# Optimization experiments

Hardware: AMD Instinct MI355X
Metric: run time of the kernel (lower is better)

Reference implementation:

```python
import jax, jax.numpy as jnp
import numpy as np

EPS = 1e-8
NUM_HEADS = 4


def setup_inputs() -> dict:
    key = jax.random.key(0)
    ks = jax.random.split(key, 20)
    N, D = 8192, 200      # total nodes, gnn/text dim
    B = 4                  # graphs (text batch)
    E, DEG = 4096, 16      # hyperedges, nodes per hyperedge
    H = 128                # fusion hidden dim
    f = lambda k, s: jax.random.normal(k, s, dtype=jnp.float32) * 0.05
    return {
        "x": jax.random.normal(ks[0], (N, D), dtype=jnp.float32),
        "text": jax.random.normal(ks[1], (B, D), dtype=jnp.float32),
        "W": f(ks[2], (D, D)),
        "b": jnp.zeros((D,), jnp.float32),
        "gate_w": f(ks[3], (D, 1)),
        "gate_b": jnp.zeros((1,), jnp.float32),
        "gnn_w": f(ks[4], (D, H)), "gnn_b": f(ks[5], (H,)),
        "text_w": f(ks[6], (D, H)), "text_b": f(ks[7], (H,)),
        "in_w": f(ks[8], (H, 3 * H)), "in_b": f(ks[9], (3 * H,)),
        "attn_out_w": f(ks[10], (H, H)), "attn_out_b": f(ks[11], (H,)),
        "fgate_w": f(ks[12], (2 * H, H)), "fgate_b": f(ks[13], (H,)),
        "outp_w": f(ks[14], (H, D)), "outp_b": f(ks[15], (D,)),
        "edge_nodes": jax.random.randint(ks[16], (E, DEG), 0, N),
    }


def _forward(x, text, W, b, gate_w, gate_b, gnn_w, gnn_b, text_w, text_b,
             in_w, in_b, attn_out_w, attn_out_b, fgate_w, fgate_b,
             outp_w, outp_b, edge_nodes):
    N, D = x.shape
    E, DEG = edge_nodes.shape
    # --- HypergraphConv: incidence build + normalized Laplacian propagation ---
    out = x @ W                                         # [N, D]
    # H[node, edge] = 1/len(edge); duplicates overwrite (set), as in torch loop
    Hinc = jnp.zeros((N, E), x.dtype).at[edge_nodes, jnp.arange(E)[:, None]].set(1.0 / DEG)
    Dv = Hinc.sum(axis=1)                               # node degree [N]
    De = Hinc.sum(axis=0)                               # edge degree [E]
    dv = 1.0 / jnp.sqrt(Dv + EPS)
    de = 1.0 / (De + EPS)
    Hl = Hinc * dv[:, None]                             # Dv^-1/2 H
    L = (Hl * de[None, :]) @ Hl.T                       # Dv^-1/2 H De^-1 H^T Dv^-1/2
    hyper_out = L @ out                                 # [N, D]
    alpha = jax.nn.sigmoid(x.mean(axis=0, keepdims=True) @ gate_w + gate_b)  # [1,1]
    gnn_feat = alpha * out + (1.0 - alpha) * hyper_out + b
    # --- CrossModalAttentionFusion on per-graph node features (3D path) ---
    B = text.shape[0]
    Nn = N // B
    gnn3 = gnn_feat.reshape(B, Nn, D)
    gp = gnn3 @ gnn_w + gnn_b                           # [B, Nn, H]
    tp = (text @ text_w + text_b)[:, None, :]           # [B, 1, H]
    Hd = gp.shape[-1]
    hd = Hd // NUM_HEADS
    q = gp @ in_w[:, :Hd] + in_b[:Hd]
    k = tp @ in_w[:, Hd:2 * Hd] + in_b[Hd:2 * Hd]
    v = tp @ in_w[:, 2 * Hd:] + in_b[2 * Hd:]
    qh = q.reshape(B, Nn, NUM_HEADS, hd).transpose(0, 2, 1, 3)   # [B,h,Nn,hd]
    kh = k.reshape(B, 1, NUM_HEADS, hd).transpose(0, 2, 1, 3)    # [B,h,1,hd]
    vh = v.reshape(B, 1, NUM_HEADS, hd).transpose(0, 2, 1, 3)
    scores = jnp.einsum("bhqd,bhkd->bhqk", qh, kh) / jnp.sqrt(jnp.float32(hd))
    attn = jax.nn.softmax(scores, axis=-1)              # kv_len=1 -> ones
    att = jnp.einsum("bhqk,bhkd->bhqd", attn, vh)
    att = att.transpose(0, 2, 1, 3).reshape(B, Nn, Hd) @ attn_out_w + attn_out_b
    g = jax.nn.sigmoid(jnp.concatenate([gp, att], axis=-1) @ fgate_w + fgate_b)
    fused = g * gp + (1.0 - g) * att
    return fused @ outp_w + outp_b                      # [B, Nn, D]


def reference(x, text, W, b, gate_w, gate_b, gnn_w, gnn_b, text_w, text_b,
              in_w, in_b, attn_out_w, attn_out_b, fgate_w, fgate_b,
              outp_w, outp_b, edge_nodes):
    return _forward(x, text, W, b, gate_w, gate_b, gnn_w, gnn_b, text_w, text_b,
                    in_w, in_b, attn_out_w, attn_out_b, fgate_w, fgate_b,
                    outp_w, outp_b, edge_nodes)
```

## Files before the change

kernel.cpp:

```cpp
#include <hip/hip_runtime.h>
#include <hip/hip_bf16.h>

#define NODES 8192
#define DIM   200
#define NEDGE 4096
#define DEGREE 16
#define NB    4
#define NNODE 2048
#define HD    128
#define MT    8
#define ECAP  32

__device__ __forceinline__ float dv_of(int cnt) {
    return 1.0f / sqrtf((float)cnt * (1.0f / 16.0f) + 1e-8f);
}

__global__ void k_front(const float* __restrict__ x, const int* __restrict__ en,
                        const float* __restrict__ W, const float* __restrict__ gnn_w,
                        const float* __restrict__ bias, const float* __restrict__ gnn_b,
                        const float* __restrict__ text, const float* __restrict__ text_w,
                        const float* __restrict__ text_b, const float* __restrict__ in_w,
                        const float* __restrict__ in_b, const float* __restrict__ aow,
                        const float* __restrict__ aob, const float* __restrict__ fgw,
                        const float* __restrict__ fgb, float* __restrict__ colsum,
                        int* __restrict__ cnt, int* __restrict__ emask,
                        int* __restrict__ elist2, float* __restrict__ Wg,
                        float* __restrict__ bg, float* __restrict__ attO,
                        float* __restrict__ attg) {
    __shared__ float st[DIM];
    __shared__ float part[2][HD];
    __shared__ float vin[HD];
    int b = blockIdx.x, t = threadIdx.x;
    if (b < 256) {
        if (t < DIM) {
            float acc = 0.f;
            int r0 = b * 32;
            for (int r = 0; r < 32; r++) acc += x[(r0 + r) * DIM + t];
            atomicAdd(&colsum[t], acc);
        }
        return;
    }
    if (b < 272) {
        int e = (b - 256) * 256 + t;
        int idx[DEGREE];
#pragma unroll
        for (int i = 0; i < DEGREE; i++) idx[i] = en[e * DEGREE + i];
        int mask = 0;
#pragma unroll
        for (int i = 0; i < DEGREE; i++) {
            bool uniq = true;
            for (int j = 0; j < i; j++) uniq = uniq && (idx[j] != idx[i]);
            if (uniq) {
                mask |= (1 << i);
                int slot = atomicAdd(&cnt[idx[i]], 1);
                if (slot < ECAP) elist2[idx[i] * ECAP + slot] = e;
            }
        }
        emask[e] = mask;
        return;
    }
    if (b < 372) {
        int r = 2 * (b - 272) + (t >> 7);
        int c = t & 127;
        const float* vec = &W[r * DIM];
        float acc = 0.f;
        for (int k = 0; k < DIM; k++) acc += vec[k] * gnn_w[k * HD + c];
        Wg[r * HD + c] = acc;
        return;
    }
    if (b == 372) {
        if (t < HD) {
            float acc = 0.f;
            for (int k = 0; k < DIM; k++) acc += bias[k] * gnn_w[k * HD + t];
            bg[t] = acc + gnn_b[t];
        }
        return;
    }
    int g = b - 373;
    int c = t & 127, h = t >> 7;
    if (t < DIM) st[t] = text[g * DIM + t];
    __syncthreads();
    {
        float acc = 0.f;
        int k0 = h * 100;
        for (int k = k0; k < k0 + 100; k++) acc += st[k] * text_w[k * HD + c];
        part[h][c] = acc;
    }
    __syncthreads();
    if (t < HD) vin[t] = part[0][t] + part[1][t] + text_b[t];
    __syncthreads();
    {
        float acc = 0.f;
        int k0 = h * 64;
        for (int k = k0; k < k0 + 64; k++) acc += vin[k] * in_w[k * 3 * HD + 2 * HD + c];
        part[h][c] = acc;
    }
    __syncthreads();
    if (t < HD) vin[t] = part[0][t] + part[1][t] + in_b[2 * HD + t];
    __syncthreads();
    {
        float acc = 0.f;
        int k0 = h * 64;
        for (int k = k0; k < k0 + 64; k++) acc += vin[k] * aow[k * HD + c];
        part[h][c] = acc;
    }
    __syncthreads();
    if (t < HD) {
        float ao = part[0][t] + part[1][t] + aob[t];
        attO[g * HD + t] = ao;
        vin[t] = ao;
    }
    __syncthreads();
    {
        float acc = 0.f;
        int k0 = h * 64;
        for (int k = k0; k < k0 + 64; k++) acc += vin[k] * fgw[(HD + k) * HD + c];
        part[h][c] = acc;
    }
    __syncthreads();
    if (t < HD) attg[g * HD + t] = part[0][t] + part[1][t] + fgb[t];
}

__global__ void k_xwg(const float* __restrict__ x, const float* __restrict__ Wg,
                      float* __restrict__ out2, const float* __restrict__ colsum,
                      const float* __restrict__ gate_w, const float* __restrict__ gate_b,
                      float* __restrict__ alpha) {
    __shared__ float sx[MT * DIM];
    int t = threadIdx.x;
    if (blockIdx.x == NODES / MT) {
        __shared__ float red[256];
        red[t] = (t < DIM) ? colsum[t] * gate_w[t] : 0.f;
        __syncthreads();
        for (int o = 128; o > 0; o >>= 1) {
            if (t < o) red[t] += red[t + o];
            __syncthreads();
        }
        if (t == 0) {
            float z = red[0] / (float)NODES + gate_b[0];
            alpha[0] = 1.0f / (1.0f + expf(-z));
        }
        return;
    }
    int bm = blockIdx.x * MT;
    const float4* x4 = (const float4*)(x + bm * DIM);
    float4* sx4 = (float4*)sx;
    for (int i = t; i < MT * DIM / 4; i += 256) sx4[i] = x4[i];
    __syncthreads();
    int c = t & 127, rg = t >> 7;
    float acc[4] = {0.f, 0.f, 0.f, 0.f};
    for (int k = 0; k < DIM; k++) {
        float w = Wg[k * HD + c];
#pragma unroll
        for (int i = 0; i < 4; i++) acc[i] += sx[(rg * 4 + i) * DIM + k] * w;
    }
#pragma unroll
    for (int i = 0; i < 4; i++) out2[(bm + rg * 4 + i) * HD + c] = acc[i];
}

__global__ void k_tE(const int* __restrict__ en, const int* __restrict__ emask,
                     const int* __restrict__ cnt, const float* __restrict__ out2,
                     float* __restrict__ tE) {
    int e = blockIdx.x * 2 + (threadIdx.x >> 7);
    int c = threadIdx.x & 127;
    int m = emask[e];
    float De = (float)__popc(m) * (1.0f / 16.0f);
    float de = 1.0f / (De + 1e-8f);
    int nd[DEGREE];
#pragma unroll
    for (int i = 0; i < DEGREE; i++) nd[i] = en[e * DEGREE + i];
    float acc = 0.f;
#pragma unroll
    for (int i = 0; i < DEGREE; i++)
        if ((m >> i) & 1) acc += dv_of(cnt[nd[i]]) * out2[nd[i] * HD + c];
    tE[e * HD + c] = de * acc;
}

__global__ void k_tail(const float* __restrict__ out2, const float* __restrict__ tE,
                       const int* __restrict__ cnt, const int* __restrict__ elist2,
                       const float* __restrict__ alpha, const float* __restrict__ bg,
                       const float* __restrict__ fgw, const float* __restrict__ attO,
                       const float* __restrict__ attg, const float* __restrict__ opw,
                       const float* __restrict__ opb, float* __restrict__ out) {
    __shared__ float sgp[MT][HD];
    __shared__ int   sid[MT][ECAP];
    __shared__ int   scount[MT];
    int bm = blockIdx.x * MT;
    int b = bm >> 11;
    int t = threadIdx.x;
    {
        int r = t >> 5, sl = t & 31;
        int n = bm + r;
        int cc = cnt[n]; cc = cc < ECAP ? cc : ECAP;
        if (sl == 0) scount[r] = cc;
        if (sl < cc) sid[r][sl] = elist2[n * ECAP + sl];
    }
    __syncthreads();
    int c = t & 127, rg = t >> 7;
    float a = alpha[0];
    float bgc = bg[c];
#pragma unroll
    for (int i = 0; i < 4; i++) {
        int r = rg * 4 + i;
        int n = bm + r;
        int cc = scount[r];
        float hyp = 0.f;
        for (int j = 0; j < cc; j++) hyp += tE[sid[r][j] * HD + c];
        hyp *= dv_of(cnt[n]) * (1.0f / 256.0f);
        sgp[r][c] = a * out2[n * HD + c] + (1.0f - a) * hyp + bgc;
    }
    __syncthreads();
    float ao = attO[b * HD + c];
    float ag = attg[b * HD + c];
    float acc[4] = {ag, ag, ag, ag};
    for (int j = 0; j < HD; j++) {
        float w = fgw[j * HD + c];
#pragma unroll
        for (int i = 0; i < 4; i++) acc[i] += sgp[rg * 4 + i][j] * w;
    }
    __syncthreads();
#pragma unroll
    for (int i = 0; i < 4; i++) {
        int r = rg * 4 + i;
        float g = 1.0f / (1.0f + expf(-acc[i]));
        sgp[r][c] = g * sgp[r][c] + (1.0f - g) * ao;
    }
    __syncthreads();
    if (t < DIM) {
        float accO[MT];
        float ob = opb[t];
#pragma unroll
        for (int i = 0; i < MT; i++) accO[i] = ob;
        for (int j = 0; j < HD; j++) {
            float w = opw[j * DIM + t];
#pragma unroll
            for (int i = 0; i < MT; i++) accO[i] += sgp[i][j] * w;
        }
#pragma unroll
        for (int i = 0; i < MT; i++) out[(bm + i) * DIM + t] = accO[i];
    }
}

extern "C" void kernel_launch(void* const* d_in, const int* in_sizes, int n_in,
                              void* d_out, int out_size, void* d_ws, size_t ws_size,
                              hipStream_t stream) {
    const float* x      = (const float*)d_in[0];
    const float* text   = (const float*)d_in[1];
    const float* W      = (const float*)d_in[2];
    const float* bias   = (const float*)d_in[3];
    const float* gate_w = (const float*)d_in[4];
    const float* gate_b = (const float*)d_in[5];
    const float* gnn_w  = (const float*)d_in[6];
    const float* gnn_b  = (const float*)d_in[7];
    const float* text_w = (const float*)d_in[8];
    const float* text_b = (const float*)d_in[9];
    const float* in_w   = (const float*)d_in[10];
    const float* in_b   = (const float*)d_in[11];
    const float* aow    = (const float*)d_in[12];
    const float* aob    = (const float*)d_in[13];
    const float* fgw    = (const float*)d_in[14];
    const float* fgb    = (const float*)d_in[15];
    const float* opw    = (const float*)d_in[16];
    const float* opb    = (const float*)d_in[17];
    const int*   en     = (const int*)d_in[18];
    float* out = (float*)d_out;

    char* p = (char*)d_ws;
    int*   cnt    = (int*)p;   p += NODES * sizeof(int);
    float* colsum = (float*)p; p += DIM * sizeof(float);
    float* out2   = (float*)p; p += (size_t)NODES * HD * sizeof(float);
    float* tE     = (float*)p; p += (size_t)NEDGE * HD * sizeof(float);
    int*   elist2 = (int*)p;   p += (size_t)NODES * ECAP * sizeof(int);
    float* Wg     = (float*)p; p += DIM * HD * sizeof(float);
    float* alpha  = (float*)p; p += sizeof(float);
    float* bg     = (float*)p; p += HD * sizeof(float);
    float* attO   = (float*)p; p += NB * HD * sizeof(float);
    float* attg   = (float*)p; p += NB * HD * sizeof(float);
    int*   emask  = (int*)p;   p += NEDGE * sizeof(int);

    hipMemsetAsync(cnt, 0, (NODES + DIM) * sizeof(int), stream);

    k_front<<<377, 256, 0, stream>>>(x, en, W, gnn_w, bias, gnn_b, text, text_w,
                                     text_b, in_w, in_b, aow, aob, fgw, fgb,
                                     colsum, cnt, emask, elist2, Wg, bg, attO, attg);
    k_xwg<<<NODES / MT + 1, 256, 0, stream>>>(x, Wg, out2, colsum, gate_w, gate_b, alpha);
    k_tE<<<NEDGE / 2, 256, 0, stream>>>(en, emask, cnt, out2, tE);
    k_tail<<<NODES / MT, 256, 0, stream>>>(out2, tE, cnt, elist2, alpha, bg, fgw,
                                           attO, attg, opw, opb, out);
}
```

Measured before the change: 168.5 us.

## Fuse four kernels into one persistent kernel with global atomic barriers

Replaces the four separate launches with a single persistent kernel of 512 blocks that walks through the stages and separates them with software grid barriers built on agent-scope atomics. The cnt array is now zeroed inside the kernel. colsum atomics are replaced by per-block partial sums that block 0 reduces. Each block handles two node tiles and eight edges per stage. The aim is to remove launch gaps and the larger memset, at the cost of barrier spin overhead and a dependence on all 512 blocks being resident at once.

```diff
diff --git a/kernel.cpp b/kernel.cpp
--- a/kernel.cpp
+++ b/kernel.cpp
@@ -1,50 +1,132 @@
 #include <hip/hip_runtime.h>
-#include <hip/hip_bf16.h>
 
 #define NODES 8192
 #define DIM   200
 #define NEDGE 4096
 #define DEGREE 16
-#define NB    4
-#define NNODE 2048
 #define HD    128
 #define MT    8
 #define ECAP  32
+#define NBLK  512
+#define NTILE (NODES / MT)
+
+struct Params {
+    const float *x, *text, *W, *bias, *gate_w, *gate_b, *gnn_w, *gnn_b,
+                *text_w, *text_b, *in_w, *in_b, *aow, *aob, *fgw, *fgb,
+                *opw, *opb;
+    const int  *en;
+    float *out;
+    int   *bar;
+    int   *cnt;
+    float *cpart;
+    float *out2;
+    float *tE;
+    int   *elist2;
+    float *Wg;
+    float *alpha;
+    float *bg;
+    float *attO;
+    float *attg;
+    int   *emask;
+};
 
 __device__ __forceinline__ float dv_of(int cnt) {
     return 1.0f / sqrtf((float)cnt * (1.0f / 16.0f) + 1e-8f);
 }
 
-__global__ void k_front(const float* __restrict__ x, const int* __restrict__ en,
-                        const float* __restrict__ W, const float* __restrict__ gnn_w,
-                        const float* __restrict__ bias, const float* __restrict__ gnn_b,
-                        const float* __restrict__ text, const float* __restrict__ text_w,
-                        const float* __restrict__ text_b, const float* __restrict__ in_w,
-                        const float* __restrict__ in_b, const float* __restrict__ aow,
-                        const float* __restrict__ aob, const float* __restrict__ fgw,
-                        const float* __restrict__ fgb, float* __restrict__ colsum,
-                        int* __restrict__ cnt, int* __restrict__ emask,
-                        int* __restrict__ elist2, float* __restrict__ Wg,
-                        float* __restrict__ bg, float* __restrict__ attO,
-                        float* __restrict__ attg) {
-    __shared__ float st[DIM];
-    __shared__ float part[2][HD];
-    __shared__ float vin[HD];
-    int b = blockIdx.x, t = threadIdx.x;
+__device__ __forceinline__ void gbar(int* bar, int idx) {
+    __syncthreads();
+    if (threadIdx.x == 0) {
+        __hip_atomic_fetch_add(&bar[idx], 1, __ATOMIC_RELEASE, __HIP_MEMORY_SCOPE_AGENT);
+        while (__hip_atomic_load(&bar[idx], __ATOMIC_RELAXED, __HIP_MEMORY_SCOPE_AGENT) < NBLK)
+            __builtin_amdgcn_s_sleep(2);
+    }
+    __syncthreads();
+    __threadfence();
+}
+
+__global__ __launch_bounds__(256, 4) void k_fused(Params p) {
+    __shared__ __align__(16) union SM {
+        float sx[MT * DIM];
+        struct { float st[DIM]; float part[2][HD]; float vin[HD]; } tx;
+        struct { float sgp[MT][HD]; int sid[MT][ECAP]; int scount[MT]; } tl;
+    } sm;
+    __shared__ float red[256];
+    const int b = blockIdx.x, t = threadIdx.x;
+
+    if (t < 16) p.cnt[b * 16 + t] = 0;
     if (b < 256) {
         if (t < DIM) {
             float acc = 0.f;
             int r0 = b * 32;
-            for (int r = 0; r < 32; r++) acc += x[(r0 + r) * DIM + t];
-            atomicAdd(&colsum[t], acc);
-        }
-        return;
-    }
-    if (b < 272) {
-        int e = (b - 256) * 256 + t;
+            for (int r = 0; r < 32; r++) acc += p.x[(r0 + r) * DIM + t];
+            p.cpart[b * DIM + t] = acc;
+        }
+    } else if (b < 356) {
+        int r = 2 * (b - 256) + (t >> 7), c = t & 127;
+        const float* vec = &p.W[r * DIM];
+        float acc = 0.f;
+        for (int k = 0; k < DIM; k++) acc += vec[k] * p.gnn_w[k * HD + c];
+        p.Wg[r * HD + c] = acc;
+    } else if (b == 356) {
+        if (t < HD) {
+            float acc = 0.f;
+            for (int k = 0; k < DIM; k++) acc += p.bias[k] * p.gnn_w[k * HD + t];
+            p.bg[t] = acc + p.gnn_b[t];
+        }
+    } else if (b < 361) {
+        int g = b - 357;
+        int c = t & 127, h = t >> 7;
+        if (t < DIM) sm.tx.st[t] = p.text[g * DIM + t];
+        __syncthreads();
+        {
+            float acc = 0.f;
+            int k0 = h * 100;
+            for (int k = k0; k < k0 + 100; k++) acc += sm.tx.st[k] * p.text_w[k * HD + c];
+            sm.tx.part[h][c] = acc;
+        }
+        __syncthreads();
+        if (t < HD) sm.tx.vin[t] = sm.tx.part[0][t] + sm.tx.part[1][t] + p.text_b[t];
+        __syncthreads();
+        {
+            float acc = 0.f;
+            int k0 = h * 64;
+            for (int k = k0; k < k0 + 64; k++)
+                acc += sm.tx.vin[k] * p.in_w[k * 3 * HD + 2 * HD + c];
+            sm.tx.part[h][c] = acc;
+        }
+        __syncthreads();
+        if (t < HD) sm.tx.vin[t] = sm.tx.part[0][t] + sm.tx.part[1][t] + p.in_b[2 * HD + t];
+        __syncthreads();
+        {
+            float acc = 0.f;
+            int k0 = h * 64;
+            for (int k = k0; k < k0 + 64; k++) acc += sm.tx.vin[k] * p.aow[k * HD + c];
+            sm.tx.part[h][c] = acc;
+        }
+        __syncthreads();
+        if (t < HD) {
+            float ao = sm.tx.part[0][t] + sm.tx.part[1][t] + p.aob[t];
+            p.attO[g * HD + t] = ao;
+            sm.tx.vin[t] = ao;
+        }
+        __syncthreads();
+        {
+            float acc = 0.f;
+            int k0 = h * 64;
+            for (int k = k0; k < k0 + 64; k++) acc += sm.tx.vin[k] * p.fgw[(HD + k) * HD + c];
+            sm.tx.part[h][c] = acc;
+        }
+        __syncthreads();
+        if (t < HD) p.attg[g * HD + t] = sm.tx.part[0][t] + sm.tx.part[1][t] + p.fgb[t];
+    }
+    gbar(p.bar, 0);
+
+    if (t < 8) {
+        int e = b * 8 + t;
         int idx[DEGREE];
 #pragma unroll
-        for (int i = 0; i < DEGREE; i++) idx[i] = en[e * DEGREE + i];
+        for (int i = 0; i < DEGREE; i++) idx[i] = p.en[e * DEGREE + i];
         int mask = 0;
 #pragma unroll
         for (int i = 0; i < DEGREE; i++) {
@@ -52,238 +134,164 @@
             for (int j = 0; j < i; j++) uniq = uniq && (idx[j] != idx[i]);
             if (uniq) {
                 mask |= (1 << i);
-                int slot = atomicAdd(&cnt[idx[i]], 1);
-                if (slot < ECAP) elist2[idx[i] * ECAP + slot] = e;
+                int slot = atomicAdd(&p.cnt[idx[i]], 1);
+                if (slot < ECAP) p.elist2[idx[i] * ECAP + slot] = e;
             }
         }
-        emask[e] = mask;
-        return;
-    }
-    if (b < 372) {
-        int r = 2 * (b - 272) + (t >> 7);
-        int c = t & 127;
-        const float* vec = &W[r * DIM];
-        float acc = 0.f;
-        for (int k = 0; k < DIM; k++) acc += vec[k] * gnn_w[k * HD + c];
-        Wg[r * HD + c] = acc;
-        return;
-    }
-    if (b == 372) {
-        if (t < HD) {
-            float acc = 0.f;
-            for (int k = 0; k < DIM; k++) acc += bias[k] * gnn_w[k * HD + t];
-            bg[t] = acc + gnn_b[t];
-        }
-        return;
-    }
-    int g = b - 373;
-    int c = t & 127, h = t >> 7;
-    if (t < DIM) st[t] = text[g * DIM + t];
-    __syncthreads();
-    {
-        float acc = 0.f;
-        int k0 = h * 100;
-        for (int k = k0; k < k0 + 100; k++) acc += st[k] * text_w[k * HD + c];
-        part[h][c] = acc;
-    }
-    __syncthreads();
-    if (t < HD) vin[t] = part[0][t] + part[1][t] + text_b[t];
-    __syncthreads();
-    {
-        float acc = 0.f;
-        int k0 = h * 64;
-        for (int k = k0; k < k0 + 64; k++) acc += vin[k] * in_w[k * 3 * HD + 2 * HD + c];
-        part[h][c] = acc;
-    }
-    __syncthreads();
-    if (t < HD) vin[t] = part[0][t] + part[1][t] + in_b[2 * HD + t];
-    __syncthreads();
-    {
-        float acc = 0.f;
-        int k0 = h * 64;
-        for (int k = k0; k < k0 + 64; k++) acc += vin[k] * aow[k * HD + c];
-        part[h][c] = acc;
-    }
-    __syncthreads();
-    if (t < HD) {
-        float ao = part[0][t] + part[1][t] + aob[t];
-        attO[g * HD + t] = ao;
-        vin[t] = ao;
-    }
-    __syncthreads();
-    {
-        float acc = 0.f;
-        int k0 = h * 64;
-        for (int k = k0; k < k0 + 64; k++) acc += vin[k] * fgw[(HD + k) * HD + c];
-        part[h][c] = acc;
-    }
-    __syncthreads();
-    if (t < HD) attg[g * HD + t] = part[0][t] + part[1][t] + fgb[t];
-}
-
-__global__ void k_xwg(const float* __restrict__ x, const float* __restrict__ Wg,
-                      float* __restrict__ out2, const float* __restrict__ colsum,
-                      const float* __restrict__ gate_w, const float* __restrict__ gate_b,
-                      float* __restrict__ alpha) {
-    __shared__ float sx[MT * DIM];
-    int t = threadIdx.x;
-    if (blockIdx.x == NODES / MT) {
-        __shared__ float red[256];
-        red[t] = (t < DIM) ? colsum[t] * gate_w[t] : 0.f;
+        p.emask[e] = mask;
+    }
+    for (int it = 0; it < 2; ++it) {
+        int bm = (b + it * NBLK) * MT;
+        const float4* x4 = (const float4*)(p.x + bm * DIM);
+        float4* sx4 = (float4*)sm.sx;
+        for (int i = t; i < MT * DIM / 4; i += 256) sx4[i] = x4[i];
+        __syncthreads();
+        int c = t & 127, rg = t >> 7;
+        float acc[4] = {0.f, 0.f, 0.f, 0.f};
+        for (int k = 0; k < DIM; k++) {
+            float w = p.Wg[k * HD + c];
+#pragma unroll
+            for (int i = 0; i < 4; i++) acc[i] += sm.sx[(rg * 4 + i) * DIM + k] * w;
+        }
+#pragma unroll
+        for (int i = 0; i < 4; i++) p.out2[(bm + rg * 4 + i) * HD + c] = acc[i];
+        __syncthreads();
+    }
+    if (b == 0) {
+        float v = 0.f;
+        if (t < DIM) {
+            float s = 0.f;
+            for (int q = 0; q < 256; q++) s += p.cpart[q * DIM + t];
+            v = s * p.gate_w[t];
+        }
+        red[t] = v;
         __syncthreads();
         for (int o = 128; o > 0; o >>= 1) {
             if (t < o) red[t] += red[t + o];
             __syncthreads();
         }
         if (t == 0) {
-            float z = red[0] / (float)NODES + gate_b[0];
-            alpha[0] = 1.0f / (1.0f + expf(-z));
-        }
-        return;
-    }
-    int bm = blockIdx.x * MT;
-    const float4* x4 = (const float4*)(x + bm * DIM);
-    float4* sx4 = (float4*)sx;
-    for (int i = t; i < MT * DIM / 4; i += 256) sx4[i] = x4[i];
-    __syncthreads();
-    int c = t & 127, rg = t >> 7;
-    float acc[4] = {0.f, 0.f, 0.f, 0.f};
-    for (int k = 0; k < DIM; k++) {
-        float w = Wg[k * HD + c];
-#pragma unroll
-        for (int i = 0; i < 4; i++) acc[i] += sx[(rg * 4 + i) * DIM + k] * w;
-    }
-#pragma unroll
-    for (int i = 0; i < 4; i++) out2[(bm + rg * 4 + i) * HD + c] = acc[i];
-}
-
-__global__ void k_tE(const int* __restrict__ en, const int* __restrict__ emask,
-                     const int* __restrict__ cnt, const float* __restrict__ out2,
-                     float* __restrict__ tE) {
-    int e = blockIdx.x * 2 + (threadIdx.x >> 7);
-    int c = threadIdx.x & 127;
-    int m = emask[e];
-    float De = (float)__popc(m) * (1.0f / 16.0f);
-    float de = 1.0f / (De + 1e-8f);
-    int nd[DEGREE];
-#pragma unroll
-    for (int i = 0; i < DEGREE; i++) nd[i] = en[e * DEGREE + i];
-    float acc = 0.f;
-#pragma unroll
-    for (int i = 0; i < DEGREE; i++)
-        if ((m >> i) & 1) acc += dv_of(cnt[nd[i]]) * out2[nd[i] * HD + c];
-    tE[e * HD + c] = de * acc;
-}
-
-__global__ void k_tail(const float* __restrict__ out2, const float* __restrict__ tE,
-                       const int* __restrict__ cnt, const int* __restrict__ elist2,
-                       const float* __restrict__ alpha, const float* __restrict__ bg,
-                       const float* __restrict__ fgw, const float* __restrict__ attO,
-                       const float* __restrict__ attg, const float* __restrict__ opw,
-                       const float* __restrict__ opb, float* __restrict__ out) {
-    __shared__ float sgp[MT][HD];
-    __shared__ int   sid[MT][ECAP];
-    __shared__ int   scount[MT];
-    int bm = blockIdx.x * MT;
-    int b = bm >> 11;
-    int t = threadIdx.x;
-    {
-        int r = t >> 5, sl = t & 31;
-        int n = bm + r;
-        int cc = cnt[n]; cc = cc < ECAP ? cc : ECAP;
-        if (sl == 0) scount[r] = cc;
-        if (sl < cc) sid[r][sl] = elist2[n * ECAP + sl];
-    }
-    __syncthreads();
-    int c = t & 127, rg = t >> 7;
-    float a = alpha[0];
-    float bgc = bg[c];
-#pragma unroll
-    for (int i = 0; i < 4; i++) {
-        int r = rg * 4 + i;
-        int n = bm + r;
-        int cc = scount[r];
-        float hyp = 0.f;
-        for (int j = 0; j < cc; j++) hyp += tE[sid[r][j] * HD + c];
-        hyp *= dv_of(cnt[n]) * (1.0f / 256.0f);
-        sgp[r][c] = a * out2[n * HD + c] + (1.0f - a) * hyp + bgc;
-    }
-    __syncthreads();
-    float ao = attO[b * HD + c];
-    float ag = attg[b * HD + c];
-    float acc[4] = {ag, ag, ag, ag};
-    for (int j = 0; j < HD; j++) {
-        float w = fgw[j * HD + c];
-#pragma unroll
-        for (int i = 0; i < 4; i++) acc[i] += sgp[rg * 4 + i][j] * w;
-    }
-    __syncthreads();
-#pragma unroll
-    for (int i = 0; i < 4; i++) {
-        int r = rg * 4 + i;
-        float g = 1.0f / (1.0f + expf(-acc[i]));
-        sgp[r][c] = g * sgp[r][c] + (1.0f - g) * ao;
-    }
-    __syncthreads();
-    if (t < DIM) {
-        float accO[MT];
-        float ob = opb[t];
-#pragma unroll
-        for (int i = 0; i < MT; i++) accO[i] = ob;
+            float z = red[0] / (float)NODES + p.gate_b[0];
+            p.alpha[0] = 1.0f / (1.0f + expf(-z));
+        }
+    }
+    gbar(p.bar, 1);
+
+#pragma unroll
+    for (int pass = 0; pass < 4; ++pass) {
+        int e = b * 8 + pass * 2 + (t >> 7);
+        int c = t & 127;
+        int m = p.emask[e];
+        float De = (float)__popc(m) * (1.0f / 16.0f);
+        float de = 1.0f / (De + 1e-8f);
+        int nd[DEGREE];
+#pragma unroll
+        for (int i = 0; i < DEGREE; i++) nd[i] = p.en[e * DEGREE + i];
+        float acc = 0.f;
+#pragma unroll
+        for (int i = 0; i < DEGREE; i++)
+            if ((m >> i) & 1) acc += dv_of(p.cnt[nd[i]]) * p.out2[nd[i] * HD + c];
+        p.tE[e * HD + c] = de * acc;
+    }
+    gbar(p.bar, 2);
+
+    for (int it = 0; it < 2; ++it) {
+        int bm = (b + it * NBLK) * MT;
+        int gb = bm >> 11;
+        {
+            int r = t >> 5, sl = t & 31;
+            int n = bm + r;
+            int cc = p.cnt[n]; cc = cc < ECAP ? cc : ECAP;
+            if (sl == 0) sm.tl.scount[r] = cc;
+            if (sl < cc) sm.tl.sid[r][sl] = p.elist2[n * ECAP + sl];
+        }
+        __syncthreads();
+        int c = t & 127, rg = t >> 7;
+        float a = p.alpha[0];
+        float bgc = p.bg[c];
+#pragma unroll
+        for (int i = 0; i < 4; i++) {
+            int r = rg * 4 + i;
+            int n = bm + r;
+            int cc = sm.tl.scount[r];
+            float hyp = 0.f;
+            for (int j = 0; j < cc; j++) hyp += p.tE[sm.tl.sid[r][j] * HD + c];
+            hyp *= dv_of(p.cnt[n]) * (1.0f / 256.0f);
+            sm.tl.sgp[r][c] = a * p.out2[n * HD + c] + (1.0f - a) * hyp + bgc;
+        }
+        __syncthreads();
+        float ao = p.attO[gb * HD + c];
+        float ag = p.attg[gb * HD + c];
+        float acc[4] = {ag, ag, ag, ag};
         for (int j = 0; j < HD; j++) {
-            float w = opw[j * DIM + t];
-#pragma unroll
-            for (int i = 0; i < MT; i++) accO[i] += sgp[i][j] * w;
-        }
-#pragma unroll
-        for (int i = 0; i < MT; i++) out[(bm + i) * DIM + t] = accO[i];
+            float w = p.fgw[j * HD + c];
+#pragma unroll
+            for (int i = 0; i < 4; i++) acc[i] += sm.tl.sgp[rg * 4 + i][j] * w;
+        }
+        __syncthreads();
+#pragma unroll
+        for (int i = 0; i < 4; i++) {
+            int r = rg * 4 + i;
+            float g = 1.0f / (1.0f + expf(-acc[i]));
+            sm.tl.sgp[r][c] = g * sm.tl.sgp[r][c] + (1.0f - g) * ao;
+        }
+        __syncthreads();
+        if (t < DIM) {
+            float accO[MT];
+            float ob = p.opb[t];
+#pragma unroll
+            for (int i = 0; i < MT; i++) accO[i] = ob;
+            for (int j = 0; j < HD; j++) {
+                float w = p.opw[j * DIM + t];
+#pragma unroll
+                for (int i = 0; i < MT; i++) accO[i] += sm.tl.sgp[i][j] * w;
+            }
+#pragma unroll
+            for (int i = 0; i < MT; i++) p.out[(bm + i) * DIM + t] = accO[i];
+        }
+        __syncthreads();
     }
 }
 
 extern "C" void kernel_launch(void* const* d_in, const int* in_sizes, int n_in,
                               void* d_out, int out_size, void* d_ws, size_t ws_size,
                               hipStream_t stream) {
-    const float* x      = (const float*)d_in[0];
-    const float* text   = (const float*)d_in[1];
-    const float* W      = (const float*)d_in[2];
-    const float* bias   = (const float*)d_in[3];
-    const float* gate_w = (const float*)d_in[4];
-    const float* gate_b = (const float*)d_in[5];
-    const float* gnn_w  = (const float*)d_in[6];
-    const float* gnn_b  = (const float*)d_in[7];
-    const float* text_w = (const float*)d_in[8];
-    const float* text_b = (const float*)d_in[9];
-    const float* in_w   = (const float*)d_in[10];
-    const float* in_b   = (const float*)d_in[11];
-    const float* aow    = (const float*)d_in[12];
-    const float* aob    = (const float*)d_in[13];
-    const float* fgw    = (const float*)d_in[14];
-    const float* fgb    = (const float*)d_in[15];
-    const float* opw    = (const float*)d_in[16];
-    const float* opb    = (const float*)d_in[17];
-    const int*   en     = (const int*)d_in[18];
-    float* out = (float*)d_out;
-
-    char* p = (char*)d_ws;
-    int*   cnt    = (int*)p;   p += NODES * sizeof(int);
-    float* colsum = (float*)p; p += DIM * sizeof(float);
-    float* out2   = (float*)p; p += (size_t)NODES * HD * sizeof(float);
-    float* tE     = (float*)p; p += (size_t)NEDGE * HD * sizeof(float);
-    int*   elist2 = (int*)p;   p += (size_t)NODES * ECAP * sizeof(int);
-    float* Wg     = (float*)p; p += DIM * HD * sizeof(float);
-    float* alpha  = (float*)p; p += sizeof(float);
-    float* bg     = (float*)p; p += HD * sizeof(float);
-    float* attO   = (float*)p; p += NB * HD * sizeof(float);
-    float* attg   = (float*)p; p += NB * HD * sizeof(float);
-    int*   emask  = (int*)p;   p += NEDGE * sizeof(int);
-
-    hipMemsetAsync(cnt, 0, (NODES + DIM) * sizeof(int), stream);
-
-    k_front<<<377, 256, 0, stream>>>(x, en, W, gnn_w, bias, gnn_b, text, text_w,
-                                     text_b, in_w, in_b, aow, aob, fgw, fgb,
-                                     colsum, cnt, emask, elist2, Wg, bg, attO, attg);
-    k_xwg<<<NODES / MT + 1, 256, 0, stream>>>(x, Wg, out2, colsum, gate_w, gate_b, alpha);
-    k_tE<<<NEDGE / 2, 256, 0, stream>>>(en, emask, cnt, out2, tE);
-    k_tail<<<NODES / MT, 256, 0, stream>>>(out2, tE, cnt, elist2, alpha, bg, fgw,
-                                           attO, attg, opw, opb, out);
-}
+    Params P;
+    P.x      = (const float*)d_in[0];
+    P.text   = (const float*)d_in[1];
+    P.W      = (const float*)d_in[2];
+    P.bias   = (const float*)d_in[3];
+    P.gate_w = (const float*)d_in[4];
+    P.gate_b = (const float*)d_in[5];
+    P.gnn_w  = (const float*)d_in[6];
+    P.gnn_b  = (const float*)d_in[7];
+    P.text_w = (const float*)d_in[8];
+    P.text_b = (const float*)d_in[9];
+    P.in_w   = (const float*)d_in[10];
+    P.in_b   = (const float*)d_in[11];
+    P.aow    = (const float*)d_in[12];
+    P.aob    = (const float*)d_in[13];
+    P.fgw    = (const float*)d_in[14];
+    P.fgb    = (const float*)d_in[15];
+    P.opw    = (const float*)d_in[16];
+    P.opb    = (const float*)d_in[17];
+    P.en     = (const int*)d_in[18];
+    P.out    = (float*)d_out;
+
+    char* q = (char*)d_ws;
+    P.bar    = (int*)q;   q += 4 * sizeof(int);
+    P.cnt    = (int*)q;   q += NODES * sizeof(int);
+    P.cpart  = (float*)q; q += 256 * DIM * sizeof(float);
+    P.out2   = (float*)q; q += (size_t)NODES * HD * sizeof(float);
+    P.tE     = (float*)q; q += (size_t)NEDGE * HD * sizeof(float);
+    P.elist2 = (int*)q;   q += (size_t)NODES * ECAP * sizeof(int);
+    P.Wg     = (float*)q; q += DIM * HD * sizeof(float);
+    P.alpha  = (float*)q; q += sizeof(float);
+    P.bg     = (float*)q; q += HD * sizeof(float);
+    P.attO   = (float*)q; q += 4 * HD * sizeof(float);
+    P.attg   = (float*)q; q += 4 * HD * sizeof(float);
+    P.emask  = (int*)q;   q += NEDGE * sizeof(int);
+
+    hipMemsetAsync(d_ws, 0, 16, stream);
+    hipLaunchKernelGGL(k_fused, dim3(NBLK), dim3(256), 0, stream, P);
+}
```

Result: slower. 380.2 us (+125.6%).

## Drop memset, move incidence build into xwg kernel, retile node GEMM

Applied to the files above, without the earlier changes.

Removes the hipMemsetAsync by zeroing the count array inside k_front, and replaces the atomic column-sum with per-block partial sums that the alpha block reduces. The hyperedge dedup/incidence-list construction moves from k_front into k_xwg, where the first 8 threads of each block handle 8 edges while the block also computes a 16-row tile of x·Wg (each thread now covers 4 rows × 2 columns). The aim is to cut one launch, avoid atomics on colsum, and raise per-thread reuse in the GEMM. The trade-off is halved block count in k_xwg and a serialized edge-processing prologue on a few lanes before the GEMM.

```diff
diff --git a/kernel.cpp b/kernel.cpp
--- a/kernel.cpp
+++ b/kernel.cpp
@@ -1,12 +1,9 @@
 #include <hip/hip_runtime.h>
-#include <hip/hip_bf16.h>
 
 #define NODES 8192
 #define DIM   200
 #define NEDGE 4096
 #define DEGREE 16
-#define NB    4
-#define NNODE 2048
 #define HD    128
 #define MT    8
 #define ECAP  32
@@ -15,33 +12,123 @@
     return 1.0f / sqrtf((float)cnt * (1.0f / 16.0f) + 1e-8f);
 }
 
-__global__ void k_front(const float* __restrict__ x, const int* __restrict__ en,
-                        const float* __restrict__ W, const float* __restrict__ gnn_w,
-                        const float* __restrict__ bias, const float* __restrict__ gnn_b,
-                        const float* __restrict__ text, const float* __restrict__ text_w,
-                        const float* __restrict__ text_b, const float* __restrict__ in_w,
-                        const float* __restrict__ in_b, const float* __restrict__ aow,
-                        const float* __restrict__ aob, const float* __restrict__ fgw,
-                        const float* __restrict__ fgb, float* __restrict__ colsum,
-                        int* __restrict__ cnt, int* __restrict__ emask,
-                        int* __restrict__ elist2, float* __restrict__ Wg,
-                        float* __restrict__ bg, float* __restrict__ attO,
-                        float* __restrict__ attg) {
+__global__ void k_front(const float* __restrict__ x, const float* __restrict__ W,
+                        const float* __restrict__ gnn_w, const float* __restrict__ bias,
+                        const float* __restrict__ gnn_b, const float* __restrict__ text,
+                        const float* __restrict__ text_w, const float* __restrict__ text_b,
+                        const float* __restrict__ in_w, const float* __restrict__ in_b,
+                        const float* __restrict__ aow, const float* __restrict__ aob,
+                        const float* __restrict__ fgw, const float* __restrict__ fgb,
+                        float* __restrict__ cpart, int* __restrict__ cnt,
+                        float* __restrict__ Wg, float* __restrict__ bg,
+                        float* __restrict__ attO, float* __restrict__ attg) {
     __shared__ float st[DIM];
     __shared__ float part[2][HD];
     __shared__ float vin[HD];
     int b = blockIdx.x, t = threadIdx.x;
     if (b < 256) {
+        if (t < 32) cnt[b * 32 + t] = 0;
         if (t < DIM) {
             float acc = 0.f;
             int r0 = b * 32;
             for (int r = 0; r < 32; r++) acc += x[(r0 + r) * DIM + t];
-            atomicAdd(&colsum[t], acc);
+            cpart[b * DIM + t] = acc;
         }
         return;
     }
-    if (b < 272) {
-        int e = (b - 256) * 256 + t;
+    if (b < 356) {
+        int r = 2 * (b - 256) + (t >> 7);
+        int c = t & 127;
+        const float* vec = &W[r * DIM];
+        float acc = 0.f;
+        for (int k = 0; k < DIM; k++) acc += vec[k] * gnn_w[k * HD + c];
+        Wg[r * HD + c] = acc;
+        return;
+    }
+    if (b == 356) {
+        if (t < HD) {
+            float acc = 0.f;
+            for (int k = 0; k < DIM; k++) acc += bias[k] * gnn_w[k * HD + t];
+            bg[t] = acc + gnn_b[t];
+        }
+        return;
+    }
+    int g = b - 357;
+    int c = t & 127, h = t >> 7;
+    if (t < DIM) st[t] = text[g * DIM + t];
+    __syncthreads();
+    {
+        float acc = 0.f;
+        int k0 = h * 100;
+        for (int k = k0; k < k0 + 100; k++) acc += st[k] * text_w[k * HD + c];
+        part[h][c] = acc;
+    }
+    __syncthreads();
+    if (t < HD) vin[t] = part[0][t] + part[1][t] + text_b[t];
+    __syncthreads();
+    {
+        float acc = 0.f;
+        int k0 = h * 64;
+        for (int k = k0; k < k0 + 64; k++) acc += vin[k] * in_w[k * 3 * HD + 2 * HD + c];
+        part[h][c] = acc;
+    }
+    __syncthreads();
+    if (t < HD) vin[t] = part[0][t] + part[1][t] + in_b[2 * HD + t];
+    __syncthreads();
+    {
+        float acc = 0.f;
+        int k0 = h * 64;
+        for (int k = k0; k < k0 + 64; k++) acc += vin[k] * aow[k * HD + c];
+        part[h][c] = acc;
+    }
+    __syncthreads();
+    if (t < HD) {
+        float ao = part[0][t] + part[1][t] + aob[t];
+        attO[g * HD + t] = ao;
+        vin[t] = ao;
+    }
+    __syncthreads();
+    {
+        float acc = 0.f;
+        int k0 = h * 64;
+        for (int k = k0; k < k0 + 64; k++) acc += vin[k] * fgw[(HD + k) * HD + c];
+        part[h][c] = acc;
+    }
+    __syncthreads();
+    if (t < HD) attg[g * HD + t] = part[0][t] + part[1][t] + fgb[t];
+}
+
+__global__ void k_xwg(const float* __restrict__ x, const float* __restrict__ Wg,
+                      const int* __restrict__ en, float* __restrict__ out2,
+                      int* __restrict__ cnt, int* __restrict__ emask,
+                      int* __restrict__ elist2, const float* __restrict__ cpart,
+                      const float* __restrict__ gate_w, const float* __restrict__ gate_b,
+                      float* __restrict__ alpha) {
+    __shared__ float sx[16 * DIM];
+    int t = threadIdx.x;
+    if (blockIdx.x == 512) {
+        __shared__ float red[256];
+        float v = 0.f;
+        if (t < DIM) {
+            float s = 0.f;
+            for (int q = 0; q < 256; q++) s += cpart[q * DIM + t];
+            v = s * gate_w[t];
+        }
+        red[t] = v;
+        __syncthreads();
+        for (int o = 128; o > 0; o >>= 1) {
+            if (t < o) red[t] += red[t + o];
+            __syncthreads();
+        }
+        if (t == 0) {
+            float z = red[0] / (float)NODES + gate_b[0];
+            alpha[0] = 1.0f / (1.0f + expf(-z));
+        }
+        return;
+    }
+    int b = blockIdx.x;
+    if (t < 8) {
+        int e = b * 8 + t;
         int idx[DEGREE];
 #pragma unroll
         for (int i = 0; i < DEGREE; i++) idx[i] = en[e * DEGREE + i];
@@ -57,104 +144,30 @@
             }
         }
         emask[e] = mask;
-        return;
-    }
-    if (b < 372) {
-        int r = 2 * (b - 272) + (t >> 7);
-        int c = t & 127;
-        const float* vec = &W[r * DIM];
-        float acc = 0.f;
-        for (int k = 0; k < DIM; k++) acc += vec[k] * gnn_w[k * HD + c];
-        Wg[r * HD + c] = acc;
-        return;
-    }
-    if (b == 372) {
-        if (t < HD) {
-            float acc = 0.f;
-            for (int k = 0; k < DIM; k++) acc += bias[k] * gnn_w[k * HD + t];
-            bg[t] = acc + gnn_b[t];
-        }
-        return;
-    }
-    int g = b - 373;
-    int c = t & 127, h = t >> 7;
-    if (t < DIM) st[t] = text[g * DIM + t];
-    __syncthreads();
-    {
-        float acc = 0.f;
-        int k0 = h * 100;
-        for (int k = k0; k < k0 + 100; k++) acc += st[k] * text_w[k * HD + c];
-        part[h][c] = acc;
-    }
-    __syncthreads();
-    if (t < HD) vin[t] = part[0][t] + part[1][t] + text_b[t];
-    __syncthreads();
-    {
-        float acc = 0.f;
-        int k0 = h * 64;
-        for (int k = k0; k < k0 + 64; k++) acc += vin[k] * in_w[k * 3 * HD + 2 * HD + c];
-        part[h][c] = acc;
-    }
-    __syncthreads();
-    if (t < HD) vin[t] = part[0][t] + part[1][t] + in_b[2 * HD + t];
-    __syncthreads();
-    {
-        float acc = 0.f;
-        int k0 = h * 64;
-        for (int k = k0; k < k0 + 64; k++) acc += vin[k] * aow[k * HD + c];
-        part[h][c] = acc;
-    }
-    __syncthreads();
-    if (t < HD) {
-        float ao = part[0][t] + part[1][t] + aob[t];
-        attO[g * HD + t] = ao;
-        vin[t] = ao;
-    }
-    __syncthreads();
-    {
-        float acc = 0.f;
-        int k0 = h * 64;
-        for (int k = k0; k < k0 + 64; k++) acc += vin[k] * fgw[(HD + k) * HD + c];
-        part[h][c] = acc;
-    }
-    __syncthreads();
-    if (t < HD) attg[g * HD + t] = part[0][t] + part[1][t] + fgb[t];
-}
-
-__global__ void k_xwg(const float* __restrict__ x, const float* __restrict__ Wg,
-                      float* __restrict__ out2, const float* __restrict__ colsum,
-                      const float* __restrict__ gate_w, const float* __restrict__ gate_b,
-                      float* __restrict__ alpha) {
-    __shared__ float sx[MT * DIM];
-    int t = threadIdx.x;
-    if (blockIdx.x == NODES / MT) {
-        __shared__ float red[256];
-        red[t] = (t < DIM) ? colsum[t] * gate_w[t] : 0.f;
-        __syncthreads();
-        for (int o = 128; o > 0; o >>= 1) {
-            if (t < o) red[t] += red[t + o];
-            __syncthreads();
-        }
-        if (t == 0) {
-            float z = red[0] / (float)NODES + gate_b[0];
-            alpha[0] = 1.0f / (1.0f + expf(-z));
-        }
-        return;
-    }
-    int bm = blockIdx.x * MT;
+    }
+    int bm = b * 16;
     const float4* x4 = (const float4*)(x + bm * DIM);
     float4* sx4 = (float4*)sx;
-    for (int i = t; i < MT * DIM / 4; i += 256) sx4[i] = x4[i];
-    __syncthreads();
-    int c = t & 127, rg = t >> 7;
-    float acc[4] = {0.f, 0.f, 0.f, 0.f};
+    for (int i = t; i < 16 * DIM / 4; i += 256) sx4[i] = x4[i];
+    __syncthreads();
+    int rg = t >> 6;
+    int c0 = t & 63;
+    float acc[4][2] = {{0.f,0.f},{0.f,0.f},{0.f,0.f},{0.f,0.f}};
     for (int k = 0; k < DIM; k++) {
-        float w = Wg[k * HD + c];
-#pragma unroll
-        for (int i = 0; i < 4; i++) acc[i] += sx[(rg * 4 + i) * DIM + k] * w;
-    }
-#pragma unroll
-    for (int i = 0; i < 4; i++) out2[(bm + rg * 4 + i) * HD + c] = acc[i];
+        float w0 = Wg[k * HD + c0];
+        float w1 = Wg[k * HD + c0 + 64];
+#pragma unroll
+        for (int i = 0; i < 4; i++) {
+            float s = sx[(rg * 4 + i) * DIM + k];
+            acc[i][0] += s * w0;
+            acc[i][1] += s * w1;
+        }
+    }
+#pragma unroll
+    for (int i = 0; i < 4; i++) {
+        out2[(bm + rg * 4 + i) * HD + c0]      = acc[i][0];
+        out2[(bm + rg * 4 + i) * HD + c0 + 64] = acc[i][1];
+    }
 }
 
 __global__ void k_tE(const int* __restrict__ en, const int* __restrict__ emask,
@@ -264,25 +277,24 @@
     const int*   en     = (const int*)d_in[18];
     float* out = (float*)d_out;
 
-    char* p = (char*)d_ws;
-    int*   cnt    = (int*)p;   p += NODES * sizeof(int);
-    float* colsum = (float*)p; p += DIM * sizeof(float);
-    float* out2   = (float*)p; p += (size_t)NODES * HD * sizeof(float);
-    float* tE     = (float*)p; p += (size_t)NEDGE * HD * sizeof(float);
-    int*   elist2 = (int*)p;   p += (size_t)NODES * ECAP * sizeof(int);
-    float* Wg     = (float*)p; p += DIM * HD * sizeof(float);
-    float* alpha  = (float*)p; p += sizeof(float);
-    float* bg     = (float*)p; p += HD * sizeof(float);
-    float* attO   = (float*)p; p += NB * HD * sizeof(float);
-    float* attg   = (float*)p; p += NB * HD * sizeof(float);
-    int*   emask  = (int*)p;   p += NEDGE * sizeof(int);
-
-    hipMemsetAsync(cnt, 0, (NODES + DIM) * sizeof(int), stream);
-
-    k_front<<<377, 256, 0, stream>>>(x, en, W, gnn_w, bias, gnn_b, text, text_w,
-                                     text_b, in_w, in_b, aow, aob, fgw, fgb,
-                                     colsum, cnt, emask, elist2, Wg, bg, attO, attg);
-    k_xwg<<<NODES / MT + 1, 256, 0, stream>>>(x, Wg, out2, colsum, gate_w, gate_b, alpha);
+    char* q = (char*)d_ws;
+    int*   cnt    = (int*)q;   q += NODES * sizeof(int);
+    float* cpart  = (float*)q; q += 256 * DIM * sizeof(float);
+    float* out2   = (float*)q; q += (size_t)NODES * HD * sizeof(float);
+    float* tE     = (float*)q; q += (size_t)NEDGE * HD * sizeof(float);
+    int*   elist2 = (int*)q;   q += (size_t)NODES * ECAP * sizeof(int);
+    float* Wg     = (float*)q; q += DIM * HD * sizeof(float);
+    float* alpha  = (float*)q; q += sizeof(float);
+    float* bg     = (float*)q; q += HD * sizeof(float);
+    float* attO   = (float*)q; q += 4 * HD * sizeof(float);
+    float* attg   = (float*)q; q += 4 * HD * sizeof(float);
+    int*   emask  = (int*)q;   q += NEDGE * sizeof(int);
+
+    k_front<<<361, 256, 0, stream>>>(x, W, gnn_w, bias, gnn_b, text, text_w, text_b,
+                                     in_w, in_b, aow, aob, fgw, fgb,
+                                     cpart, cnt, Wg, bg, attO, attg);
+    k_xwg<<<513, 256, 0, stream>>>(x, Wg, en, out2, cnt, emask, elist2,
+                                   cpart, gate_w, gate_b, alpha);
     k_tE<<<NEDGE / 2, 256, 0, stream>>>(en, emask, cnt, out2, tE);
     k_tail<<<NODES / MT, 256, 0, stream>>>(out2, tE, cnt, elist2, alpha, bg, fgw,
                                            attO, attg, opw, opb, out);
```

After: 160.9 us. 4.5% less time.
